# Performance work log

Hardware: AMD Instinct MI355X
Metric: run time of the kernel (lower is better)

## Reference

```python
import jax, jax.numpy as jnp
import numpy as np

L, B, T, N, C, H, K, M = 2, 4, 8, 2048, 2, 64, 3, 32
DIN0, DIN1, DOUT = C + H, 2 * H, 4 * H


def setup_inputs() -> dict:
    key = jax.random.key(0)
    ks = jax.random.split(key, 24)
    s = 0.05
    p = lambda k, shape: jax.random.normal(k, shape, jnp.float32) * s
    return {
        # support matrices, roughly row-normalized random graph
        "G": jax.random.uniform(ks[0], (K, N, N), jnp.float32) * (2.0 / N),
        "x_seq": jax.random.normal(ks[1], (B, T, N, C), jnp.float32),
        "init_h": jnp.zeros((L, B, N, H), jnp.float32),
        "init_c": jnp.zeros((L, B, N, H), jnp.float32),
        "x_meta": jax.random.normal(ks[2], (B, T, M), jnp.float32),
        # layer 0 meta-learner params (dim_in = C+H)
        "lw1_0": p(ks[3], (M, 64)), "lb1_0": p(ks[4], (64,)),
        "lw2_0": p(ks[5], (64, K * DIN0 * DOUT)), "lb2_0": p(ks[6], (K * DIN0 * DOUT,)),
        "bw1_0": p(ks[7], (M, 64)), "bb1_0": p(ks[8], (64,)),
        "bw2_0": p(ks[9], (64, DOUT)), "bb2_0": p(ks[10], (DOUT,)),
        # layer 1 meta-learner params (dim_in = 2H)
        "lw1_1": p(ks[11], (M, 64)), "lb1_1": p(ks[12], (64,)),
        "lw2_1": p(ks[13], (64, K * DIN1 * DOUT)), "lb2_1": p(ks[14], (K * DIN1 * DOUT,)),
        "bw1_1": p(ks[15], (M, 64)), "bb1_1": p(ks[16], (64,)),
        "bw2_1": p(ks[17], (64, DOUT)), "bb2_1": p(ks[18], (DOUT,)),
    }


def _meta_gcn(G, x, meta, lw1, lb1, lw2, lb2, bw1, bb1, bw2, bb2):
    # x: [B, N, din] -> out: [B, N, 4H]
    Bb, Nn, din = x.shape
    # K-hop supports, concatenated along feature dim (k-major, matches torch.cat)
    sup = jnp.einsum('kij,bjd->bikd', G, x).reshape(Bb, Nn, K * din)
    W = (jax.nn.relu(meta @ lw1 + lb1) @ lw2 + lb2).reshape(Bb, K * din, DOUT)
    b = (jax.nn.relu(meta @ bw1 + bb1) @ bw2 + bb2)[:, None, :]
    return jnp.einsum('bnd,bdo->bno', sup, W) + b


def _run_layer(G, xs_t, meta_t, h0, c0, params):
    # xs_t: [T, B, N, din_x], meta_t: [T, B, M]
    def step(carry, inp):
        h, c = carry
        x_t, m_t = inp
        conv = _meta_gcn(G, jnp.concatenate([x_t, h], axis=-1), m_t, *params)
        gi, gf, go, gg = jnp.split(conv, 4, axis=-1)
        c_t = jax.nn.sigmoid(gf) * c + jax.nn.sigmoid(gi) * jnp.tanh(gg)
        h_t = jax.nn.sigmoid(go) * jnp.tanh(c_t)
        return (h_t, c_t), h_t
    (hT, cT), hs = jax.lax.scan(step, (h0, c0), (xs_t, meta_t))
    return hT, cT, hs


def reference(G, x_seq, init_h, init_c, x_meta,
              lw1_0, lb1_0, lw2_0, lb2_0, bw1_0, bb1_0, bw2_0, bb2_0,
              lw1_1, lb1_1, lw2_1, lb2_1, bw1_1, bb1_1, bw2_1, bb2_1):
    xs = jnp.transpose(x_seq, (1, 0, 2, 3))      # [T, B, N, C]
    ms = jnp.transpose(x_meta, (1, 0, 2))        # [T, B, M]
    p0 = (lw1_0, lb1_0, lw2_0, lb2_0, bw1_0, bb1_0, bw2_0, bb2_0)
    p1 = (lw1_1, lb1_1, lw2_1, lb2_1, bw1_1, bb1_1, bw2_1, bb2_1)
    h0T, c0T, hs0 = _run_layer(G, xs, ms, init_h[0], init_c[0], p0)
    h1T, c1T, _ = _run_layer(G, hs0, ms, init_h[1], init_c[1], p1)
    # [2, L, B, N, H]: [final h per layer; final c per layer]
    return jnp.stack([jnp.stack([h0T, h1T]), jnp.stack([c0T, c1T])])
```

## Files before the change

kernel.cpp:

```cpp
#include <hip/hip_runtime.h>
#include <hip/hip_bf16.h>
#include <cstdint>


typedef __hip_bfloat16 bf16;
typedef __attribute__((ext_vector_type(8))) short bf16x8;
typedef __attribute__((ext_vector_type(4))) short s16x4;
typedef __attribute__((ext_vector_type(4)))  float f32x4;
typedef __attribute__((ext_vector_type(16))) float f32x16;
typedef __attribute__((ext_vector_type(4)))  int   i32x4;
typedef __attribute__((ext_vector_type(16))) int   i32x16;

__device__ __forceinline__ short f2bf(float f) {
    unsigned u = __builtin_bit_cast(unsigned, f);
    return (short)((u + 0x7fffu + ((u >> 16) & 1u)) >> 16);
}

#define GLD_LDS(gaddr, laddr)                                                  \
    __builtin_amdgcn_global_load_lds(                                          \
        (const __attribute__((address_space(1))) void*)(gaddr),                \
        (__attribute__((address_space(3))) void*)(laddr), 16, 0, 0)

#define OFF_GSW    0u
#define OFF_GI8    25165824u
#define OFF_HFA0   37748736u
#define OFF_HFA1   38273024u
#define OFF_HFB0   38797312u
#define OFF_HFB1   39321600u
#define OFF_XS0T   39845888u
#define OFF_HS0T   40370176u
#define OFF_S0X    48758784u
#define OFF_S1S    49545216u
#define OFF_W0SW   74711040u
#define OFF_W1SW   79429632u
#define OFF_BIAS0  85721088u
#define OFF_BIAS1  85753856u
#define OFF_C0     85786624u
#define OFF_C1     87883776u
#define WS_NEEDED  89980928u

__global__ __launch_bounds__(256) void prep_kernel(
    const float* __restrict__ G, const float* __restrict__ x_seq,
    const float* __restrict__ init_h, const float* __restrict__ init_c,
    bf16* __restrict__ Gsw, long* __restrict__ Gi8,
    long* __restrict__ hfA0, long* __restrict__ hfA1,
    bf16* __restrict__ Xs0T, float* __restrict__ c0, float* __restrict__ c1)
{
    const int T_GSB = 1572864;
    const int T_GI8 = 1572864;
    const int T_HF  = 131072;
    const int T_XS  = 262144;
    const int T_C   = 1048576;
    const int TOTAL = T_GSB + T_GI8 + T_HF + T_XS + T_C;
    int stride = gridDim.x * 256;
    for (int idx = blockIdx.x*256 + threadIdx.x; idx < TOTAL; idx += stride) {
        int i0 = idx;
        if (i0 < T_GSB) {
            int lane = i0 & 63, jc = (i0 >> 6) & 127, it32 = (i0 >> 13) & 63, k = i0 >> 19;
            int row = it32*32 + (lane & 31);
            int col = jc*16 + (lane >> 5)*8;
            const float* gp = G + ((size_t)(k*2048 + row))*2048 + col;
            f32x4 v0 = *(const f32x4*)gp, v1 = *(const f32x4*)(gp + 4);
            bf16x8 o;
            #pragma unroll
            for (int e = 0; e < 4; e++) { o[e] = f2bf(v0[e]); o[e+4] = f2bf(v1[e]); }
            *(bf16x8*)((short*)Gsw + (size_t)i0*8) = o;
            continue;
        }
        i0 -= T_GSB;
        if (i0 < T_GI8) {
            int lane = i0 & 63, jc = (i0 >> 6) & 127, it32 = (i0 >> 13) & 63, k = i0 >> 19;
            int row = it32*32 + (lane & 31);
            int col = jc*16 + (lane >> 5)*8;
            const float* gp = G + ((size_t)(k*2048 + row))*2048 + col;
            f32x4 v0 = *(const f32x4*)gp, v1 = *(const f32x4*)(gp + 4);
            long r = 0;
            #pragma unroll
            for (int e = 0; e < 4; e++) {
                int q0 = __float2int_rn(v0[e] * 130048.0f);
                int q1 = __float2int_rn(v1[e] * 130048.0f);
                q0 = q0 < 0 ? 0 : (q0 > 127 ? 127 : q0);
                q1 = q1 < 0 ? 0 : (q1 > 127 ? 127 : q1);
                r |= ((long)(unsigned char)(char)q0) << (8*e);
                r |= ((long)(unsigned char)(char)q1) << (8*(e+4));
            }
            Gi8[i0] = r;
            continue;
        }
        i0 -= T_GI8;
        if (i0 < T_HF) {
            int lane = i0 & 63, dc = (i0 >> 6) & 1, jc = (i0 >> 7) & 127;
            int b = (i0 >> 14) & 3, L = i0 >> 16;
            int j0 = jc*16 + (lane >> 5)*8, d = dc*32 + (lane & 31);
            long r = 0;
            #pragma unroll
            for (int e = 0; e < 8; e++) {
                float hv = init_h[((size_t)(L*4 + b)*2048 + j0 + e)*64 + d];
                int q = __float2int_rn(hv * 127.0f);
                q = q < -127 ? -127 : (q > 127 ? 127 : q);
                r |= ((long)(unsigned char)(char)q) << (8*e);
            }
            long* dst = (L == 0) ? hfA0 : hfA1;
            dst[i0 & 65535] = r;
            continue;
        }
        i0 -= T_HF;
        if (i0 < T_XS) {
            int n = i0 >> 11, j = i0 & 2047;
            float v = 0.f;
            if (n < 64) {
                int t = n >> 3, rm = n & 7, b = rm >> 1, cc = rm & 1;
                v = x_seq[(((size_t)b*8 + t)*2048 + j)*2 + cc];
            }
            Xs0T[i0] = __float2bfloat16(v);
            continue;
        }
        i0 -= T_XS;
        if (i0 < 524288) { c0[i0] = init_c[i0]; continue; }
        i0 -= 524288;
        c1[i0] = init_c[524288 + i0];
    }
}

__global__ __launch_bounds__(256) void metaw_kernel(
    const float* __restrict__ x_meta,
    const float* __restrict__ lw1_0, const float* __restrict__ lb1_0,
    const float* __restrict__ lw2_0, const float* __restrict__ lb2_0,
    const float* __restrict__ bw1_0, const float* __restrict__ bb1_0,
    const float* __restrict__ bw2_0, const float* __restrict__ bb2_0,
    const float* __restrict__ lw1_1, const float* __restrict__ lb1_1,
    const float* __restrict__ lw2_1, const float* __restrict__ lb2_1,
    const float* __restrict__ bw1_1, const float* __restrict__ bb1_1,
    const float* __restrict__ bw2_1, const float* __restrict__ bb2_1,
    bf16* __restrict__ W0sw, bf16* __restrict__ W1sw,
    float* __restrict__ bias0, float* __restrict__ bias1)
{
    int tid = threadIdx.x, bid = blockIdx.x;
    const float *w1, *b1v, *w2, *b2v;
    int task, r = 0;
    if (bid < 384)      { task = 0; r = bid;       w1=lw1_1; b1v=lb1_1; w2=lw2_1; b2v=lb2_1; }
    else if (bid < 582) { task = 1; r = bid - 384; w1=lw1_0; b1v=lb1_0; w2=lw2_0; b2v=lb2_0; }
    else if (bid == 582){ task = 2;                w1=bw1_0; b1v=bb1_0; w2=bw2_0; b2v=bb2_0; }
    else                { task = 3;                w1=bw1_1; b1v=bb1_1; w2=bw2_1; b2v=bb2_1; }

    __shared__ float hid[32][64];
    for (int idx = tid; idx < 2048; idx += 256) {
        int tb = idx >> 6, h = idx & 63;
        int tt = tb >> 2, b = tb & 3;
        float a = b1v[h];
        #pragma unroll
        for (int m = 0; m < 32; m++)
            a += x_meta[((size_t)b*8 + tt)*32 + m] * w1[m*64 + h];
        hid[tb][h] = fmaxf(a, 0.f);
    }
    __syncthreads();

    int o = tid;
    int RO = (task == 0) ? 98304 : (task == 1) ? 50688 : 256;
    int ro = (task >= 2) ? o : (r*256 + o);
    float col[64];
    #pragma unroll
    for (int h = 0; h < 64; h++) col[h] = w2[(size_t)h*RO + ro];
    float base = b2v[ro];

    for (int tb = 0; tb < 32; tb++) {
        float v = base;
        #pragma unroll
        for (int h = 0; h < 64; h++) v += hid[tb][h]*col[h];
        if (task == 0) {
            int rp = r, rc = rp >> 5, rr = rp & 31;
            int oc = o >> 4, l = ((rr >> 3) << 4) + (o & 15), e = rr & 7;
            W1sw[(((size_t)tb*12 + rc)*16 + oc)*512 + l*8 + e] = __float2bfloat16(v);
        } else if (task == 1) {
            int k = r/66, d = r - k*66;
            int rp = k*96 + (d < 2 ? 64 + d : d - 2);
            int rc = rp >> 5, rr = rp & 31;
            int oc = o >> 4, l = ((rr >> 3) << 4) + (o & 15), e = rr & 7;
            W0sw[(((size_t)tb*9 + rc)*16 + oc)*512 + l*8 + e] = __float2bfloat16(v);
        } else if (task == 2) bias0[tb*256 + o] = v;
        else                  bias1[tb*256 + o] = v;
    }
}

template<int MODE>
__global__ __launch_bounds__(256) void gemm_tile(
    const short* __restrict__ Gsw, const short* __restrict__ Bm,
    bf16* __restrict__ dstB)
{
    constexpr int NT  = (MODE == 1) ? 16 : 1;
    constexpr int NWG = 48 * NT;

    int bid  = blockIdx.x;
    int wgid = (bid & 7) * (NWG / 8) + (bid >> 3);
    int mt, nt;
    if (MODE == 1) { mt = wgid >> 4; nt = wgid & 15; }
    else           { mt = wgid; nt = 0; }
    int kk = mt >> 4;

    __shared__ short lB[128 * 64];

    int tid = threadIdx.x, lane = tid & 63, w = tid >> 6;
    int wr = w >> 1, wc = w & 1;
    int l31 = lane & 31, lhi = lane >> 5;

    int rloc = lane >> 3;
    int gsrc = ((lane & 7) ^ rloc) * 8;
    const short* Bb = Bm + (size_t)(nt * 128) * 2048 + gsrc;

    f32x16 acc[2][2];
    #pragma unroll
    for (int a2 = 0; a2 < 2; a2++)
        #pragma unroll
        for (int b2 = 0; b2 < 2; b2++)
            #pragma unroll
            for (int q = 0; q < 16; q++) acc[a2][b2][q] = 0.f;

    for (int kb = 0; kb < 2048; kb += 64) {
        #pragma unroll
        for (int q = 0; q < 4; q++) {
            int row = (w * 4 + q) * 8 + rloc;
            GLD_LDS(Bb + (size_t)row * 2048 + kb, &lB[(w * 4 + q) * 512]);
        }
        __syncthreads();
        #pragma unroll
        for (int ks = 0; ks < 4; ks++) {
            int jc = (kb >> 4) + ks;
            bf16x8 af[2], bf2[2];
            #pragma unroll
            for (int a2 = 0; a2 < 2; a2++) {
                int it32 = (mt & 15) * 4 + wr * 2 + a2;
                af[a2] = *(const bf16x8*)(Gsw +
                    ((((size_t)(kk * 64 + it32)) * 128 + jc) * 64 + lane) * 8);
            }
            #pragma unroll
            for (int b2 = 0; b2 < 2; b2++) {
                int r = wc * 64 + b2 * 32 + l31;
                int cb = (ks * 32 + lhi * 16) ^ ((r & 7) << 4);
                bf2[b2] = *(const bf16x8*)((const char*)lB + r * 128 + cb);
            }
            #pragma unroll
            for (int a2 = 0; a2 < 2; a2++)
                #pragma unroll
                for (int b2 = 0; b2 < 2; b2++)
                    acc[a2][b2] = __builtin_amdgcn_mfma_f32_32x32x16_bf16(
                        af[a2], bf2[b2], acc[a2][b2], 0, 0, 0);
        }
        __syncthreads();
    }

    #pragma unroll
    for (int a2 = 0; a2 < 2; a2++) {
        #pragma unroll
        for (int b2 = 0; b2 < 2; b2++) {
            int gn = nt * 128 + wc * 64 + b2 * 32 + l31;
            #pragma unroll
            for (int reg = 0; reg < 16; reg++) {
                int gm = (mt & 15) * 128 + wr * 64 + a2 * 32
                         + (reg & 3) + 8 * (reg >> 2) + 4 * lhi;
                float v = acc[a2][b2][reg];
                if (MODE == 1) {
                    int tt = gn >> 8, c = gn & 255;
                    dstB[(((size_t)tt * 3 + kk) * 2048 + gm) * 256 + c] = __float2bfloat16(v);
                } else {
                    if (gn < 64)
                        dstB[((size_t)kk * 2048 + gm) * 64 + gn] = __float2bfloat16(v);
                }
            }
        }
    }
}

#define LD(P, JC)                                                              \
    do { _Pragma("unroll") for (int k = 0; k < 3; k++)                         \
            P##a[k] = Gi8[(((size_t)(k * 64 + it)) * 128 + (JC)) * 64 + lane]; \
         _Pragma("unroll") for (int dc = 0; dc < 2; dc++)                      \
            P##b[dc] = hfr_in[(((size_t)(b * 128 + (JC))) * 2 + dc) * 64 + lane]; \
    } while (0)

#define CP(P)                                                                  \
    do { _Pragma("unroll") for (int k = 0; k < 3; k++)                         \
         _Pragma("unroll") for (int dc = 0; dc < 2; dc++)                      \
            acc6[k * 2 + dc] = __builtin_amdgcn_mfma_i32_32x32x16_i8(          \
                P##a[k], P##b[dc], acc6[k * 2 + dc], 0, 0, 0);                 \
    } while (0)

template<int LAYER>
__global__ __launch_bounds__(512, 2) void step_fused(
    const long* __restrict__ Gi8, const short* __restrict__ Sstat,
    const short* __restrict__ Wsw, const float* __restrict__ bias,
    float* __restrict__ cbuf, const long* __restrict__ hfr_in,
    long* __restrict__ hfr_out, bf16* __restrict__ hs0T,
    float* __restrict__ out, int t)
{
    constexpr int NC = (LAYER == 0) ? 9 : 12;
    __shared__ char lds[120832];
    char* SUP = lds + 98304;
    short* hT = (short*)(lds + 114688);
    char* hTq = lds + 118784;
    int* RB = (int*)lds;

    int tid = threadIdx.x, lane = tid & 63, w = tid >> 6;
    int wh = w & 3, kg = w >> 2;
    int bid = blockIdx.x;
    int q = bid >> 3;
    int it = (bid & 7) * 8 + (q >> 2), b = q & 3;
    int i0 = it * 32;
    int l31 = lane & 31, lhi = lane >> 5, l15 = lane & 15, lg = lane >> 4;

    i32x16 acc6[6];
    #pragma unroll
    for (int f = 0; f < 6; f++)
        #pragma unroll
        for (int r = 0; r < 16; r++) acc6[f][r] = 0;

    {
        int jc0 = w * 16;
        long fAa[3], fAb[2], fBa[3], fBb[2], fCa[3], fCb[2], fDa[3], fDb[2];
        LD(fA, jc0 + 0); LD(fB, jc0 + 1); LD(fC, jc0 + 2); LD(fD, jc0 + 3);
        #pragma unroll 1
        for (int j4 = 0; j4 < 3; j4++) {
            CP(fA); LD(fA, jc0 + j4 * 4 + 4);
            CP(fB); LD(fB, jc0 + j4 * 4 + 5);
            CP(fC); LD(fC, jc0 + j4 * 4 + 6);
            CP(fD); LD(fD, jc0 + j4 * 4 + 7);
        }
        CP(fA); CP(fB); CP(fC); CP(fD);
    }

    if (w >= 4) {
        #pragma unroll
        for (int f = 0; f < 6; f++)
            #pragma unroll
            for (int qq = 0; qq < 4; qq++) {
                i32x4 v;
                #pragma unroll
                for (int r = 0; r < 4; r++) v[r] = acc6[f][qq * 4 + r];
                *(i32x4*)(RB + ((size_t)((w - 4) * 6 + f)) * 1024 + lane * 16 + qq * 4) = v;
            }
    }
    __syncthreads();
    if (w < 4) {
        #pragma unroll
        for (int f = 0; f < 6; f++)
            #pragma unroll
            for (int r = 0; r < 16; r++)
                acc6[f][r] += RB[((size_t)(w * 6 + f)) * 1024 + lane * 16 + r];
    }
    __syncthreads();
    if (w == 2 || w == 3) {
        #pragma unroll
        for (int f = 0; f < 6; f++)
            #pragma unroll
            for (int qq = 0; qq < 4; qq++) {
                i32x4 v;
                #pragma unroll
                for (int r = 0; r < 4; r++) v[r] = acc6[f][qq * 4 + r];
                *(i32x4*)(RB + ((size_t)((w - 2) * 6 + f)) * 1024 + lane * 16 + qq * 4) = v;
            }
    }
    __syncthreads();
    if (w < 2) {
        #pragma unroll
        for (int f = 0; f < 6; f++)
            #pragma unroll
            for (int r = 0; r < 16; r++)
                acc6[f][r] += RB[((size_t)(w * 6 + f)) * 1024 + lane * 16 + r];
    }
    __syncthreads();
    if (w == 1) {
        #pragma unroll
        for (int f = 0; f < 6; f++)
            #pragma unroll
            for (int qq = 0; qq < 4; qq++) {
                i32x4 v;
                #pragma unroll
                for (int r = 0; r < 4; r++) v[r] = acc6[f][qq * 4 + r];
                *(i32x4*)(RB + (size_t)f * 1024 + lane * 16 + qq * 4) = v;
            }
    }
    __syncthreads();
    if (w == 0) {
        const float SCL = 1.0f / 16516096.0f;
        #pragma unroll
        for (int f = 0; f < 6; f++) {
            int k = f >> 1, dc = f & 1;
            #pragma unroll
            for (int reg = 0; reg < 16; reg++) {
                int s = acc6[f][reg] + RB[(size_t)f * 1024 + lane * 16 + reg];
                float sf = (float)s * SCL;
                int i = (reg & 3) + 8 * (reg >> 2) + 4 * lhi;
                int dpos = k * 64 + dc * 32 + l31;
                *(short*)(SUP + i * 512 + ((dpos * 2) ^ ((i & 15) << 4))) = f2bf(sf);
            }
        }
    }
    __syncthreads();

    f32x4 ag[4];
    #pragma unroll
    for (int g = 0; g < 4; g++)
        #pragma unroll
        for (int r = 0; r < 4; r++) ag[g][r] = 0.f;

    const short* WswT = Wsw + (size_t)(t * 4 + b) * NC * 16 * 512;
    int rowA = kg * 16 + l15;

    #pragma unroll
    for (int rc = 0; rc < NC; rc++) {
        bf16x8 aa;
        if (LAYER == 1) {
            int kk = rc >> 2, dq = rc & 3;
            if (dq < 2) {
                const short* src = Sstat + (size_t)t * 3 * 2048 * 256;
                int col = b * 64 + dq * 32 + lg * 8;
                aa = *(const bf16x8*)(src + ((size_t)kk * 2048 + i0 + rowA) * 256 + col);
            } else {
                int dpb = (kk * 64 + (dq - 2) * 32 + lg * 8) * 2;
                aa = *(const bf16x8*)(SUP + rowA * 512 + (dpb ^ (l15 << 4)));
            }
        } else {
            int kk = rc / 3, dd = rc - kk * 3;
            if (dd < 2) {
                int dpb = (kk * 64 + dd * 32 + lg * 8) * 2;
                aa = *(const bf16x8*)(SUP + rowA * 512 + (dpb ^ (l15 << 4)));
            } else {
                #pragma unroll
                for (int e = 0; e < 8; e++) aa[e] = 0;
                if (lg == 0) {
                    unsigned v0 = *(const unsigned*)(Sstat + ((size_t)kk * 2048 + i0 + rowA) * 64 + t * 8 + b * 2);
                    aa[0] = (short)(v0 & 0xffff); aa[1] = (short)(v0 >> 16);
                }
            }
        }
        #pragma unroll
        for (int g = 0; g < 4; g++) {
            bf16x8 wf = *(const bf16x8*)(WswT + (((size_t)rc * 16 + (g * 4 + wh)) * 64 + lane) * 8);
            ag[g] = __builtin_amdgcn_mfma_f32_16x16x32_bf16(aa, wf, ag[g], 0, 0, 0);
        }
    }

    int hcol = wh * 16 + l15;
    float bia[4];
    #pragma unroll
    for (int g = 0; g < 4; g++) bia[g] = bias[(t * 4 + b) * 256 + g * 64 + hcol];

    #pragma unroll
    for (int r = 0; r < 4; r++) {
        int iloc = kg * 16 + lg * 4 + r;
        int i = i0 + iloc;
        float gi = ag[0][r] + bia[0];
        float gf = ag[1][r] + bia[1];
        float go = ag[2][r] + bia[2];
        float gg = ag[3][r] + bia[3];
        size_t cidx = ((size_t)b * 2048 + i) * 64 + hcol;
        float c_old = cbuf[cidx];
        float si = 1.f / (1.f + __expf(-gi));
        float sf = 1.f / (1.f + __expf(-gf));
        float so = 1.f / (1.f + __expf(-go));
        float cn = sf * c_old + si * tanhf(gg);
        float hn = so * tanhf(cn);
        cbuf[cidx] = cn;
        hT[iloc * 64 + hcol] = f2bf(hn);
        int hq = __float2int_rn(hn * 127.0f);
        hq = hq < -127 ? -127 : (hq > 127 ? 127 : hq);
        hTq[iloc * 64 + hcol] = (char)hq;
        if (t == 7) {
            out[(((size_t)LAYER * 4 + b) * 2048 + i) * 64 + hcol]       = hn;
            out[(((size_t)(2 + LAYER) * 4 + b) * 2048 + i) * 64 + hcol] = cn;
        }
    }
    __syncthreads();

    if (tid < 256) {
        int jh = tid >> 7, dc = (tid >> 6) & 1, lane6 = tid & 63;
        long r = 0;
        #pragma unroll
        for (int e = 0; e < 8; e++)
            r |= ((long)(unsigned char)hTq[(jh * 16 + (lane6 >> 5) * 8 + e) * 64
                                           + dc * 32 + (lane6 & 31)]) << (8 * e);
        hfr_out[(((size_t)(b * 128 + it * 2 + jh)) * 2 + dc) * 64 + lane6] = r;
    }
    if (LAYER == 0) {
        int row = tid >> 3, seg = tid & 7;
        s16x4 v;
        #pragma unroll
        for (int u = 0; u < 4; u++) v[u] = hT[(seg * 4 + u) * 64 + row];
        short* dst = (short*)hs0T + ((size_t)t * 256 + b * 64 + row) * 2048 + i0 + seg * 4;
        *(s16x4*)dst = v;
    }
}

extern "C" void kernel_launch(void* const* d_in, const int* in_sizes, int n_in,
                              void* d_out, int out_size, void* d_ws, size_t ws_size,
                              hipStream_t stream)
{
    const float* G      = (const float*)d_in[0];
    const float* x_seq  = (const float*)d_in[1];
    const float* init_h = (const float*)d_in[2];
    const float* init_c = (const float*)d_in[3];
    const float* x_meta = (const float*)d_in[4];
    const float* lw1_0 = (const float*)d_in[5],  *lb1_0 = (const float*)d_in[6];
    const float* lw2_0 = (const float*)d_in[7],  *lb2_0 = (const float*)d_in[8];
    const float* bw1_0 = (const float*)d_in[9],  *bb1_0 = (const float*)d_in[10];
    const float* bw2_0 = (const float*)d_in[11], *bb2_0 = (const float*)d_in[12];
    const float* lw1_1 = (const float*)d_in[13], *lb1_1 = (const float*)d_in[14];
    const float* lw2_1 = (const float*)d_in[15], *lb2_1 = (const float*)d_in[16];
    const float* bw1_1 = (const float*)d_in[17], *bb1_1 = (const float*)d_in[18];
    const float* bw2_1 = (const float*)d_in[19], *bb2_1 = (const float*)d_in[20];

    if (ws_size < WS_NEEDED) return;

    char* ws = (char*)d_ws;
    bf16*  Gsw   = (bf16*) (ws + OFF_GSW);
    long*  Gi8   = (long*) (ws + OFF_GI8);
    long*  hfA0  = (long*) (ws + OFF_HFA0);
    long*  hfA1  = (long*) (ws + OFF_HFA1);
    long*  hfB0  = (long*) (ws + OFF_HFB0);
    long*  hfB1  = (long*) (ws + OFF_HFB1);
    bf16*  Xs0T  = (bf16*) (ws + OFF_XS0T);
    bf16*  hs0T  = (bf16*) (ws + OFF_HS0T);
    bf16*  S0x   = (bf16*) (ws + OFF_S0X);
    bf16*  S1s   = (bf16*) (ws + OFF_S1S);
    bf16*  W0sw  = (bf16*) (ws + OFF_W0SW);
    bf16*  W1sw  = (bf16*) (ws + OFF_W1SW);
    float* bias0 = (float*)(ws + OFF_BIAS0);
    float* bias1 = (float*)(ws + OFF_BIAS1);
    float* c0    = (float*)(ws + OFF_C0);
    float* c1    = (float*)(ws + OFF_C1);
    float* out   = (float*)d_out;

    prep_kernel<<<4096, 256, 0, stream>>>(G, x_seq, init_h, init_c,
                                          Gsw, Gi8, hfA0, hfA1, Xs0T, c0, c1);
    metaw_kernel<<<584, 256, 0, stream>>>(x_meta,
        lw1_0, lb1_0, lw2_0, lb2_0, bw1_0, bb1_0, bw2_0, bb2_0,
        lw1_1, lb1_1, lw2_1, lb2_1, bw1_1, bb1_1, bw2_1, bb2_1,
        W0sw, W1sw, bias0, bias1);

    gemm_tile<2><<<48, 256, 0, stream>>>((const short*)Gsw, (const short*)Xs0T, S0x);

    for (int t = 0; t < 8; t++) {
        const long* hin  = (t & 1) ? hfB0 : hfA0;
        long*       hout = (t & 1) ? hfA0 : hfB0;
        step_fused<0><<<256, 512, 0, stream>>>(Gi8, (const short*)S0x,
            (const short*)W0sw, bias0, c0, hin, hout, hs0T, out, t);
    }

    gemm_tile<1><<<768, 256, 0, stream>>>((const short*)Gsw, (const short*)hs0T, S1s);

    for (int t = 0; t < 8; t++) {
        const long* hin  = (t & 1) ? hfB1 : hfA1;
        long*       hout = (t & 1) ? hfA1 : hfB1;
        step_fused<1><<<256, 512, 0, stream>>>(Gi8, (const short*)S1s,
            (const short*)W1sw, bias1, c1, hin, hout, nullptr, out, t);
    }
}
```

Before: 482.5 us.

## Wavefront-pipeline both LSTM layers and the layer-1 support GEMM in one launch

Replaces the 16 sequential per-step launches plus the big layer-1 GEMM with 10 launches of a single kernel. Each launch runs layer-0 step tau, the layer-1 support GEMM for step tau-1, and layer-1 step tau-2 on disjoint block ranges, so work from the two layers overlaps. The step blocks shrink from 512 to 256 threads: each wave now covers twice the K range, which removes the cross-wave LDS reduction, and handles two row tiles in the gate GEMM. This trades fewer launches and better overlap for longer per-wave serial loops, and for many idle early-exit blocks in the first and last launches.

```diff
diff --git a/kernel.cpp b/kernel.cpp
--- a/kernel.cpp
+++ b/kernel.cpp
@@ -182,30 +182,20 @@
     }
 }
 
-template<int MODE>
-__global__ __launch_bounds__(256) void gemm_tile(
+__device__ __forceinline__ void gemm_body(
+    char* ldsbase, int mt, int ntg, int outMode ,
     const short* __restrict__ Gsw, const short* __restrict__ Bm,
     bf16* __restrict__ dstB)
 {
-    constexpr int NT  = (MODE == 1) ? 16 : 1;
-    constexpr int NWG = 48 * NT;
-
-    int bid  = blockIdx.x;
-    int wgid = (bid & 7) * (NWG / 8) + (bid >> 3);
-    int mt, nt;
-    if (MODE == 1) { mt = wgid >> 4; nt = wgid & 15; }
-    else           { mt = wgid; nt = 0; }
+    short* lB = (short*)ldsbase;
     int kk = mt >> 4;
-
-    __shared__ short lB[128 * 64];
-
     int tid = threadIdx.x, lane = tid & 63, w = tid >> 6;
     int wr = w >> 1, wc = w & 1;
     int l31 = lane & 31, lhi = lane >> 5;
 
     int rloc = lane >> 3;
     int gsrc = ((lane & 7) ^ rloc) * 8;
-    const short* Bb = Bm + (size_t)(nt * 128) * 2048 + gsrc;
+    const short* Bb = Bm + (size_t)(ntg * 128) * 2048 + gsrc;
 
     f32x16 acc[2][2];
     #pragma unroll
@@ -252,13 +242,13 @@
     for (int a2 = 0; a2 < 2; a2++) {
         #pragma unroll
         for (int b2 = 0; b2 < 2; b2++) {
-            int gn = nt * 128 + wc * 64 + b2 * 32 + l31;
+            int gn = ntg * 128 + wc * 64 + b2 * 32 + l31;
             #pragma unroll
             for (int reg = 0; reg < 16; reg++) {
                 int gm = (mt & 15) * 128 + wr * 64 + a2 * 32
                          + (reg & 3) + 8 * (reg >> 2) + 4 * lhi;
                 float v = acc[a2][b2][reg];
-                if (MODE == 1) {
+                if (outMode == 1) {
                     int tt = gn >> 8, c = gn & 255;
                     dstB[(((size_t)tt * 3 + kk) * 2048 + gm) * 256 + c] = __float2bfloat16(v);
                 } else {
@@ -270,6 +260,16 @@
     }
 }
 
+__global__ __launch_bounds__(256) void s0x_kernel(
+    const short* __restrict__ Gsw, const short* __restrict__ Bm,
+    bf16* __restrict__ dstB)
+{
+    __shared__ char lds[16384];
+    int bid = blockIdx.x;
+    int wgid = (bid & 7) * 6 + (bid >> 3);
+    gemm_body(lds, wgid, 0, 2, Gsw, Bm, dstB);
+}
+
 #define LD(P, JC)                                                              \
     do { _Pragma("unroll") for (int k = 0; k < 3; k++)                         \
             P##a[k] = Gi8[(((size_t)(k * 64 + it)) * 128 + (JC)) * 64 + lane]; \
@@ -285,25 +285,23 @@
     } while (0)
 
 template<int LAYER>
-__global__ __launch_bounds__(512, 2) void step_fused(
+__device__ __forceinline__ void step_part(
+    char* lds, int idx, int t,
     const long* __restrict__ Gi8, const short* __restrict__ Sstat,
     const short* __restrict__ Wsw, const float* __restrict__ bias,
     float* __restrict__ cbuf, const long* __restrict__ hfr_in,
     long* __restrict__ hfr_out, bf16* __restrict__ hs0T,
-    float* __restrict__ out, int t)
+    float* __restrict__ out)
 {
     constexpr int NC = (LAYER == 0) ? 9 : 12;
-    __shared__ char lds[120832];
-    char* SUP = lds + 98304;
-    short* hT = (short*)(lds + 114688);
-    char* hTq = lds + 118784;
     int* RB = (int*)lds;
+    char* SUP = lds + 49152;
+    short* hT = (short*)(lds + 65536);
+    char* hTq = lds + 69632;
 
     int tid = threadIdx.x, lane = tid & 63, w = tid >> 6;
-    int wh = w & 3, kg = w >> 2;
-    int bid = blockIdx.x;
-    int q = bid >> 3;
-    int it = (bid & 7) * 8 + (q >> 2), b = q & 3;
+    int q = idx >> 3;
+    int it = (idx & 7) * 8 + (q >> 2), b = q & 3;
     int i0 = it * 32;
     int l31 = lane & 31, lhi = lane >> 5, l15 = lane & 15, lg = lane >> 4;
 
@@ -314,11 +312,11 @@
         for (int r = 0; r < 16; r++) acc6[f][r] = 0;
 
     {
-        int jc0 = w * 16;
+        int jc0 = w * 32;
         long fAa[3], fAb[2], fBa[3], fBb[2], fCa[3], fCb[2], fDa[3], fDb[2];
         LD(fA, jc0 + 0); LD(fB, jc0 + 1); LD(fC, jc0 + 2); LD(fD, jc0 + 3);
         #pragma unroll 1
-        for (int j4 = 0; j4 < 3; j4++) {
+        for (int j4 = 0; j4 < 7; j4++) {
             CP(fA); LD(fA, jc0 + j4 * 4 + 4);
             CP(fB); LD(fB, jc0 + j4 * 4 + 5);
             CP(fC); LD(fC, jc0 + j4 * 4 + 6);
@@ -327,27 +325,7 @@
         CP(fA); CP(fB); CP(fC); CP(fD);
     }
 
-    if (w >= 4) {
-        #pragma unroll
-        for (int f = 0; f < 6; f++)
-            #pragma unroll
-            for (int qq = 0; qq < 4; qq++) {
-                i32x4 v;
-                #pragma unroll
-                for (int r = 0; r < 4; r++) v[r] = acc6[f][qq * 4 + r];
-                *(i32x4*)(RB + ((size_t)((w - 4) * 6 + f)) * 1024 + lane * 16 + qq * 4) = v;
-            }
-    }
-    __syncthreads();
-    if (w < 4) {
-        #pragma unroll
-        for (int f = 0; f < 6; f++)
-            #pragma unroll
-            for (int r = 0; r < 16; r++)
-                acc6[f][r] += RB[((size_t)(w * 6 + f)) * 1024 + lane * 16 + r];
-    }
-    __syncthreads();
-    if (w == 2 || w == 3) {
+    if (w >= 2) {
         #pragma unroll
         for (int f = 0; f < 6; f++)
             #pragma unroll
@@ -396,82 +374,92 @@
     }
     __syncthreads();
 
-    f32x4 ag[4];
-    #pragma unroll
-    for (int g = 0; g < 4; g++)
-        #pragma unroll
-        for (int r = 0; r < 4; r++) ag[g][r] = 0.f;
+    f32x4 ag[2][4];
+    #pragma unroll
+    for (int mi = 0; mi < 2; mi++)
+        #pragma unroll
+        for (int g = 0; g < 4; g++)
+            #pragma unroll
+            for (int r = 0; r < 4; r++) ag[mi][g][r] = 0.f;
 
     const short* WswT = Wsw + (size_t)(t * 4 + b) * NC * 16 * 512;
-    int rowA = kg * 16 + l15;
 
     #pragma unroll
     for (int rc = 0; rc < NC; rc++) {
-        bf16x8 aa;
+        bf16x8 a0, a1;
         if (LAYER == 1) {
             int kk = rc >> 2, dq = rc & 3;
             if (dq < 2) {
                 const short* src = Sstat + (size_t)t * 3 * 2048 * 256;
                 int col = b * 64 + dq * 32 + lg * 8;
-                aa = *(const bf16x8*)(src + ((size_t)kk * 2048 + i0 + rowA) * 256 + col);
+                a0 = *(const bf16x8*)(src + ((size_t)kk * 2048 + i0 + l15) * 256 + col);
+                a1 = *(const bf16x8*)(src + ((size_t)kk * 2048 + i0 + 16 + l15) * 256 + col);
             } else {
                 int dpb = (kk * 64 + (dq - 2) * 32 + lg * 8) * 2;
-                aa = *(const bf16x8*)(SUP + rowA * 512 + (dpb ^ (l15 << 4)));
+                a0 = *(const bf16x8*)(SUP + l15 * 512 + (dpb ^ (l15 << 4)));
+                a1 = *(const bf16x8*)(SUP + (l15 + 16) * 512 + (dpb ^ (l15 << 4)));
             }
         } else {
             int kk = rc / 3, dd = rc - kk * 3;
             if (dd < 2) {
                 int dpb = (kk * 64 + dd * 32 + lg * 8) * 2;
-                aa = *(const bf16x8*)(SUP + rowA * 512 + (dpb ^ (l15 << 4)));
+                a0 = *(const bf16x8*)(SUP + l15 * 512 + (dpb ^ (l15 << 4)));
+                a1 = *(const bf16x8*)(SUP + (l15 + 16) * 512 + (dpb ^ (l15 << 4)));
             } else {
                 #pragma unroll
-                for (int e = 0; e < 8; e++) aa[e] = 0;
+                for (int e = 0; e < 8; e++) { a0[e] = 0; a1[e] = 0; }
                 if (lg == 0) {
-                    unsigned v0 = *(const unsigned*)(Sstat + ((size_t)kk * 2048 + i0 + rowA) * 64 + t * 8 + b * 2);
-                    aa[0] = (short)(v0 & 0xffff); aa[1] = (short)(v0 >> 16);
+                    unsigned v0 = *(const unsigned*)(Sstat + ((size_t)kk * 2048 + i0 + l15) * 64 + t * 8 + b * 2);
+                    unsigned v1 = *(const unsigned*)(Sstat + ((size_t)kk * 2048 + i0 + 16 + l15) * 64 + t * 8 + b * 2);
+                    a0[0] = (short)(v0 & 0xffff); a0[1] = (short)(v0 >> 16);
+                    a1[0] = (short)(v1 & 0xffff); a1[1] = (short)(v1 >> 16);
                 }
             }
         }
         #pragma unroll
         for (int g = 0; g < 4; g++) {
-            bf16x8 wf = *(const bf16x8*)(WswT + (((size_t)rc * 16 + (g * 4 + wh)) * 64 + lane) * 8);
-            ag[g] = __builtin_amdgcn_mfma_f32_16x16x32_bf16(aa, wf, ag[g], 0, 0, 0);
-        }
-    }
-
-    int hcol = wh * 16 + l15;
+            bf16x8 wf = *(const bf16x8*)(WswT + (((size_t)rc * 16 + (g * 4 + w)) * 64 + lane) * 8);
+            ag[0][g] = __builtin_amdgcn_mfma_f32_16x16x32_bf16(a0, wf, ag[0][g], 0, 0, 0);
+            ag[1][g] = __builtin_amdgcn_mfma_f32_16x16x32_bf16(a1, wf, ag[1][g], 0, 0, 0);
+        }
+    }
+
+    int hcol = w * 16 + l15;
     float bia[4];
     #pragma unroll
     for (int g = 0; g < 4; g++) bia[g] = bias[(t * 4 + b) * 256 + g * 64 + hcol];
 
     #pragma unroll
-    for (int r = 0; r < 4; r++) {
-        int iloc = kg * 16 + lg * 4 + r;
-        int i = i0 + iloc;
-        float gi = ag[0][r] + bia[0];
-        float gf = ag[1][r] + bia[1];
-        float go = ag[2][r] + bia[2];
-        float gg = ag[3][r] + bia[3];
-        size_t cidx = ((size_t)b * 2048 + i) * 64 + hcol;
-        float c_old = cbuf[cidx];
-        float si = 1.f / (1.f + __expf(-gi));
-        float sf = 1.f / (1.f + __expf(-gf));
-        float so = 1.f / (1.f + __expf(-go));
-        float cn = sf * c_old + si * tanhf(gg);
-        float hn = so * tanhf(cn);
-        cbuf[cidx] = cn;
-        hT[iloc * 64 + hcol] = f2bf(hn);
-        int hq = __float2int_rn(hn * 127.0f);
-        hq = hq < -127 ? -127 : (hq > 127 ? 127 : hq);
-        hTq[iloc * 64 + hcol] = (char)hq;
-        if (t == 7) {
-            out[(((size_t)LAYER * 4 + b) * 2048 + i) * 64 + hcol]       = hn;
-            out[(((size_t)(2 + LAYER) * 4 + b) * 2048 + i) * 64 + hcol] = cn;
+    for (int mi = 0; mi < 2; mi++) {
+        #pragma unroll
+        for (int r = 0; r < 4; r++) {
+            int iloc = mi * 16 + lg * 4 + r;
+            int i = i0 + iloc;
+            float gi = ag[mi][0][r] + bia[0];
+            float gf = ag[mi][1][r] + bia[1];
+            float go = ag[mi][2][r] + bia[2];
+            float gg = ag[mi][3][r] + bia[3];
+            size_t cidx = ((size_t)b * 2048 + i) * 64 + hcol;
+            float c_old = cbuf[cidx];
+            float si = 1.f / (1.f + __expf(-gi));
+            float sf = 1.f / (1.f + __expf(-gf));
+            float so = 1.f / (1.f + __expf(-go));
+            float cn = sf * c_old + si * tanhf(gg);
+            float hn = so * tanhf(cn);
+            cbuf[cidx] = cn;
+            hT[iloc * 64 + hcol] = f2bf(hn);
+            int hq = __float2int_rn(hn * 127.0f);
+            hq = hq < -127 ? -127 : (hq > 127 ? 127 : hq);
+            hTq[iloc * 64 + hcol] = (char)hq;
+            if (t == 7) {
+                out[(((size_t)LAYER * 4 + b) * 2048 + i) * 64 + hcol]       = hn;
+                out[(((size_t)(2 + LAYER) * 4 + b) * 2048 + i) * 64 + hcol] = cn;
+            }
         }
     }
     __syncthreads();
 
-    if (tid < 256) {
+    {
         int jh = tid >> 7, dc = (tid >> 6) & 1, lane6 = tid & 63;
         long r = 0;
         #pragma unroll
@@ -481,12 +469,52 @@
         hfr_out[(((size_t)(b * 128 + it * 2 + jh)) * 2 + dc) * 64 + lane6] = r;
     }
     if (LAYER == 0) {
-        int row = tid >> 3, seg = tid & 7;
-        s16x4 v;
-        #pragma unroll
-        for (int u = 0; u < 4; u++) v[u] = hT[(seg * 4 + u) * 64 + row];
-        short* dst = (short*)hs0T + ((size_t)t * 256 + b * 64 + row) * 2048 + i0 + seg * 4;
-        *(s16x4*)dst = v;
+        int row = tid >> 2, seg = tid & 3;
+        bf16x8 v;
+        #pragma unroll
+        for (int u = 0; u < 8; u++) v[u] = hT[(seg * 8 + u) * 64 + row];
+        short* dst = (short*)hs0T + ((size_t)t * 256 + b * 64 + row) * 2048 + i0 + seg * 8;
+        *(bf16x8*)dst = v;
+    }
+}
+
+__global__ __launch_bounds__(256) void mega_kernel(
+    const long* __restrict__ Gi8, const short* __restrict__ Gsw,
+    const short* __restrict__ S0x, bf16* __restrict__ S1s,
+    const short* __restrict__ W0sw, const short* __restrict__ W1sw,
+    const float* __restrict__ bias0, const float* __restrict__ bias1,
+    float* __restrict__ c0, float* __restrict__ c1,
+    long* __restrict__ hfA0, long* __restrict__ hfB0,
+    long* __restrict__ hfA1, long* __restrict__ hfB1,
+    bf16* __restrict__ hs0T, float* __restrict__ out, int tau)
+{
+    __shared__ char lds[71680];
+    int bid = blockIdx.x;
+    int stripe = bid / 19, pos = bid - stripe * 19;
+
+    if (pos < 8) {
+        int t = tau;
+        if (t > 7) return;
+        int idx = stripe * 8 + pos;
+        const long* hin  = (t & 1) ? hfB0 : hfA0;
+        long*       hout = (t & 1) ? hfA0 : hfB0;
+        step_part<0>(lds, idx, t, Gi8, S0x, W0sw, bias0, c0,
+                     hin, hout, hs0T, out);
+    } else if (pos < 16) {
+        int t = tau - 2;
+        if (t < 0 || t > 7) return;
+        int idx = stripe * 8 + (pos - 8);
+        const long* hin  = (t & 1) ? hfB1 : hfA1;
+        long*       hout = (t & 1) ? hfA1 : hfB1;
+        step_part<1>(lds, idx, t, Gi8, (const short*)S1s, W1sw, bias1, c1,
+                     hin, hout, nullptr, out);
+    } else {
+        int ts = tau - 1;
+        if (ts < 0 || ts > 7) return;
+        int idx = stripe * 3 + (pos - 16);
+        int mt = idx >> 1;
+        int ntg = ts * 2 + (idx & 1);
+        gemm_body(lds, mt, ntg, 1, Gsw, (const short*)hs0T, S1s);
     }
 }
 
@@ -536,21 +564,10 @@
         lw1_1, lb1_1, lw2_1, lb2_1, bw1_1, bb1_1, bw2_1, bb2_1,
         W0sw, W1sw, bias0, bias1);
 
-    gemm_tile<2><<<48, 256, 0, stream>>>((const short*)Gsw, (const short*)Xs0T, S0x);
-
-    for (int t = 0; t < 8; t++) {
-        const long* hin  = (t & 1) ? hfB0 : hfA0;
-        long*       hout = (t & 1) ? hfA0 : hfB0;
-        step_fused<0><<<256, 512, 0, stream>>>(Gi8, (const short*)S0x,
-            (const short*)W0sw, bias0, c0, hin, hout, hs0T, out, t);
-    }
-
-    gemm_tile<1><<<768, 256, 0, stream>>>((const short*)Gsw, (const short*)hs0T, S1s);
-
-    for (int t = 0; t < 8; t++) {
-        const long* hin  = (t & 1) ? hfB1 : hfA1;
-        long*       hout = (t & 1) ? hfA1 : hfB1;
-        step_fused<1><<<256, 512, 0, stream>>>(Gi8, (const short*)S1s,
-            (const short*)W1sw, bias1, c1, hin, hout, nullptr, out, t);
-    }
-}
+    s0x_kernel<<<48, 256, 0, stream>>>((const short*)Gsw, (const short*)Xs0T, S0x);
+
+    for (int tau = 0; tau < 10; tau++)
+        mega_kernel<<<608, 256, 0, stream>>>(Gi8, (const short*)Gsw,
+            (const short*)S0x, S1s, (const short*)W0sw, (const short*)W1sw,
+            bias0, bias1, c0, c1, hfA0, hfB0, hfA1, hfB1, hs0T, out, tau);
+}
```

Result: slower. 682.2 us (+41.4%).
